# Optimization experiments

Hardware: AMD Instinct MI355X
Metric: run time of the kernel (lower is better)

The kernel has to match this reference:

```python
import jax, jax.numpy as jnp
import numpy as np

B, M, D = 2, 8192, 2
N = (64, 64)


def setup_inputs() -> dict:
    key = jax.random.key(0)
    k1, k2 = jax.random.split(key)
    # non-uniform sample points in [-0.5, 0.5)^D
    x = jax.random.uniform(k1, (B, M, D), dtype=jnp.float32) - 0.5
    f_hat = jax.random.normal(k2, (B,) + N, dtype=jnp.float32)
    return {"x": x, "f_hat": f_hat}


def reference(x, f_hat):
    # frequency index grid: cartesian product of arange(-Ni//2, Ni//2) -> [K, D]
    Ns = f_hat.shape[1:]
    grids = [jnp.arange(-(n // 2), n - n // 2, dtype=x.dtype) for n in Ns]
    inds = jnp.stack(jnp.meshgrid(*grids, indexing="ij"), axis=-1).reshape(-1, len(Ns))  # [K, D]
    # phase[b, m, k] = <inds[k], x[b, m]>
    phase = jnp.einsum("bmd,kd->bmk", x, inds)
    fourier = jnp.exp(-2j * jnp.pi * phase)  # [B, M, K] complex64 (the huge intermediate)
    fh = f_hat.reshape(f_hat.shape[0], -1).astype(fourier.dtype)  # [B, K]
    y = jnp.einsum("bmk,bk->bm", fourier, fh)  # [B, M] complex64
    return y
```

## Files before the change

kernel.cpp:

```cpp
#include <hip/hip_runtime.h>
#include <math.h>


#define TWO_PI 6.28318530717958647692f
#define BM 16384

__global__ __launch_bounds__(512) void ndft_kernel(
    const float* __restrict__ x,
    const float* __restrict__ f_hat,
    float* __restrict__ out,
    int planar)
{
    __shared__ float fh[64 * 64];
    __shared__ float part[8][64][2];

    const int t   = threadIdx.x;
    const int sub = t >> 6;
    const int lp  = t & 63;
    const int gp  = blockIdx.x * 64 + lp;
    const int b   = gp >> 13;

    {
        const float4* src = (const float4*)(f_hat + b * 4096);
        float4* dst = (float4*)fh;
        dst[t]       = src[t];
        dst[t + 512] = src[t + 512];
    }
    __syncthreads();

    const float2 xp = ((const float2*)x)[gp];
    const float x1 = xp.x, x2 = xp.y;

    float s2, c2;
    sincosf(TWO_PI * x2, &s2, &c2);
    const float wr2 = c2, wi2 = -s2;

    float s1, c1;
    sincosf(TWO_PI * x1, &s1, &c1);

    const int k1base = sub << 3;
    float Pr, Pi;
    {
        const float theta = fmaf(-TWO_PI * (float)(k1base - 32), x1,
                                 (32.0f * TWO_PI) * x2);
        sincosf(theta, &Pi, &Pr);
    }

    float yr = 0.0f, yi = 0.0f;

    for (int k1i = 0; k1i < 8; ++k1i) {
        const int k1 = k1base + k1i;
        const float4* frow = (const float4*)(fh + (k1 << 6));

        float Sr = 0.0f, Si = 0.0f;
        #pragma unroll
        for (int q = 15; q >= 0; --q) {
            const float4 f = frow[q];
            {
                const float nr = fmaf(wr2, Sr, fmaf(-wi2, Si, f.w));
                const float ni = fmaf(wr2, Si, wi2 * Sr);
                Sr = nr; Si = ni;
            }
            {
                const float nr = fmaf(wr2, Sr, fmaf(-wi2, Si, f.z));
                const float ni = fmaf(wr2, Si, wi2 * Sr);
                Sr = nr; Si = ni;
            }
            {
                const float nr = fmaf(wr2, Sr, fmaf(-wi2, Si, f.y));
                const float ni = fmaf(wr2, Si, wi2 * Sr);
                Sr = nr; Si = ni;
            }
            {
                const float nr = fmaf(wr2, Sr, fmaf(-wi2, Si, f.x));
                const float ni = fmaf(wr2, Si, wi2 * Sr);
                Sr = nr; Si = ni;
            }
        }

        yr = fmaf(Pr, Sr, fmaf(-Pi, Si, yr));
        yi = fmaf(Pr, Si, fmaf( Pi, Sr, yi));

        const float nPr = fmaf(Pr, c1,  Pi * s1);
        const float nPi = fmaf(Pi, c1, -Pr * s1);
        Pr = nPr; Pi = nPi;
    }

    part[sub][lp][0] = yr;
    part[sub][lp][1] = yi;
    __syncthreads();

    if (t < 128) {
        const int p = t >> 1, comp = t & 1;
        float s = 0.0f;
        #pragma unroll
        for (int w = 0; w < 8; ++w) s += part[w][p][comp];
        const int g = blockIdx.x * 64 + p;
        if (planar) {
            out[comp * BM + g] = s;
        } else if (comp == 0) {
            out[g] = s;
        }
    }
}

extern "C" void kernel_launch(void* const* d_in, const int* in_sizes, int n_in,
                              void* d_out, int out_size, void* d_ws, size_t ws_size,
                              hipStream_t stream) {
    const float* x     = (const float*)d_in[0];
    const float* f_hat = (const float*)d_in[1];
    float* out = (float*)d_out;

    const int planar = (out_size >= 2 * BM) ? 1 : 0;

    ndft_kernel<<<dim3(256), dim3(512), 0, stream>>>(x, f_hat, out, planar);
}
```

Before: 62.44 us.

## Replace complex Horner inner loop with Goertzel/Clenshaw real recurrence, two rows interleaved

The inner k2 sum now uses a Goertzel-style real three-term recurrence (u_n = 2cos·u_{n-1} - u_{n-2} + f) in place of complex Horner multiplication. This cuts the per-coefficient work from about four FMAs to roughly one FMA plus a subtract. The final complex value is recovered from the last two states with cos and sin. Two k1 rows are processed at once so their independent dependency chains can overlap. The Goertzel recurrence can be less numerically accurate near cos≈±1.

```diff
diff --git a/kernel.cpp b/kernel.cpp
--- a/kernel.cpp
+++ b/kernel.cpp
@@ -33,7 +33,7 @@
 
     float s2, c2;
     sincosf(TWO_PI * x2, &s2, &c2);
-    const float wr2 = c2, wi2 = -s2;
+    const float twoc = 2.0f * c2;
 
     float s1, c1;
     sincosf(TWO_PI * x1, &s1, &c1);
@@ -48,42 +48,53 @@
 
     float yr = 0.0f, yi = 0.0f;
 
-    for (int k1i = 0; k1i < 8; ++k1i) {
-        const int k1 = k1base + k1i;
-        const float4* frow = (const float4*)(fh + (k1 << 6));
+    for (int pr2 = 0; pr2 < 4; ++pr2) {
+        const int k1 = k1base + (pr2 << 1);
+        const float4* f0 = (const float4*)(fh + (k1 << 6));
+        const float4* f1 = (const float4*)(fh + ((k1 + 1) << 6));
 
-        float Sr = 0.0f, Si = 0.0f;
+        float u1a = 0.0f, u2a = 0.0f;
+        float u1b = 0.0f, u2b = 0.0f;
+
         #pragma unroll
         for (int q = 15; q >= 0; --q) {
-            const float4 f = frow[q];
+            const float4 fa = f0[q];
+            const float4 fb = f1[q];
             {
-                const float nr = fmaf(wr2, Sr, fmaf(-wi2, Si, f.w));
-                const float ni = fmaf(wr2, Si, wi2 * Sr);
-                Sr = nr; Si = ni;
+                const float A = fmaf(twoc, u1a, fa.w - u2a);
+                const float B = fmaf(twoc, A,   fa.z - u1a);
+                const float C = fmaf(twoc, B,   fa.y - A);
+                const float D = fmaf(twoc, C,   fa.x - B);
+                u2a = C; u1a = D;
             }
             {
-                const float nr = fmaf(wr2, Sr, fmaf(-wi2, Si, f.z));
-                const float ni = fmaf(wr2, Si, wi2 * Sr);
-                Sr = nr; Si = ni;
-            }
-            {
-                const float nr = fmaf(wr2, Sr, fmaf(-wi2, Si, f.y));
-                const float ni = fmaf(wr2, Si, wi2 * Sr);
-                Sr = nr; Si = ni;
-            }
-            {
-                const float nr = fmaf(wr2, Sr, fmaf(-wi2, Si, f.x));
-                const float ni = fmaf(wr2, Si, wi2 * Sr);
-                Sr = nr; Si = ni;
+                const float A = fmaf(twoc, u1b, fb.w - u2b);
+                const float B = fmaf(twoc, A,   fb.z - u1b);
+                const float C = fmaf(twoc, B,   fb.y - A);
+                const float D = fmaf(twoc, C,   fb.x - B);
+                u2b = C; u1b = D;
             }
         }
 
-        yr = fmaf(Pr, Sr, fmaf(-Pi, Si, yr));
-        yi = fmaf(Pr, Si, fmaf( Pi, Sr, yi));
+        const float Sra = fmaf(-c2, u2a, u1a);
+        const float Sia = -s2 * u2a;
+        const float Srb = fmaf(-c2, u2b, u1b);
+        const float Sib = -s2 * u2b;
 
-        const float nPr = fmaf(Pr, c1,  Pi * s1);
-        const float nPi = fmaf(Pi, c1, -Pr * s1);
-        Pr = nPr; Pi = nPi;
+        yr = fmaf(Pr, Sra, fmaf(-Pi, Sia, yr));
+        yi = fmaf(Pr, Sia, fmaf( Pi, Sra, yi));
+        {
+            const float nPr = fmaf(Pr, c1,  Pi * s1);
+            const float nPi = fmaf(Pi, c1, -Pr * s1);
+            Pr = nPr; Pi = nPi;
+        }
+        yr = fmaf(Pr, Srb, fmaf(-Pi, Sib, yr));
+        yi = fmaf(Pr, Sib, fmaf( Pi, Srb, yi));
+        {
+            const float nPr = fmaf(Pr, c1,  Pi * s1);
+            const float nPi = fmaf(Pi, c1, -Pr * s1);
+            Pr = nPr; Pi = nPi;
+        }
     }
 
     part[sub][lp][0] = yr;
```

Result: faster. 59.80 us (-4.2%).
